# Kernel optimization log

Hardware: AMD Instinct MI355X
Metric: run time of the kernel (lower is better)

The kernel has to match this reference:

```python
import jax, jax.numpy as jnp
import numpy as np

NEG_SLOPE = 0.2


def gat_layer(x_src, x_dst, src, dst, W, a_src, a_dst, b, n_dst, H, C):
    # Linear transform: [Ns, H, C] / [Nd, H, C]
    h_s = (x_src @ W).reshape(-1, H, C)
    h_d = (x_dst @ W).reshape(-1, H, C)
    # Per-edge attention logits: a . [x_i || x_j] (x_i = dst/target, x_j = src)
    e = jnp.einsum('ehc,hc->eh', h_s[src], a_src) + jnp.einsum('ehc,hc->eh', h_d[dst], a_dst)
    e = jax.nn.leaky_relu(e, NEG_SLOPE)  # [E, H]
    # Segment softmax over destination neighborhoods
    m = jax.ops.segment_max(e, dst, num_segments=n_dst)          # [Nd, H]
    ex = jnp.exp(e - m[dst])
    denom = jax.ops.segment_sum(ex, dst, num_segments=n_dst)    # [Nd, H]
    alpha = ex / denom[dst]                                      # [E, H]
    # Weighted scatter-sum aggregation
    out = jax.ops.segment_sum(alpha[:, :, None] * h_s[src], dst, num_segments=n_dst)
    return out.reshape(n_dst, H * C) + b


def setup_inputs() -> dict:
    key = jax.random.key(0)
    ks = jax.random.split(key, 16)
    N, F_IN, OUT = 200000, 602, 41
    N1, N1D, E1 = 120000, 30000, 960000
    N2D, E2 = 6000, 192000
    s = 0.05
    return {
        'x': jax.random.normal(ks[0], (N, F_IN), jnp.float32),
        'n_id1': jax.random.randint(ks[1], (N1,), 0, N),
        'res_n_id1': jax.random.randint(ks[2], (N1D,), 0, N1),
        'edge_src1': jax.random.randint(ks[3], (E1,), 0, N1),
        'edge_dst1': jax.random.randint(ks[4], (E1,), 0, N1D),
        'res_n_id2': jax.random.randint(ks[5], (N2D,), 0, N1D),
        'edge_src2': jax.random.randint(ks[6], (E2,), 0, N1D),
        'edge_dst2': jax.random.randint(ks[7], (E2,), 0, N2D),
        'W1': jax.random.normal(ks[8], (F_IN, 64), jnp.float32) * s,
        'att_src1': jax.random.normal(ks[9], (8, 8), jnp.float32) * s,
        'att_dst1': jax.random.normal(ks[10], (8, 8), jnp.float32) * s,
        'bias1': jax.random.normal(ks[11], (64,), jnp.float32) * s,
        'W2': jax.random.normal(ks[12], (64, OUT), jnp.float32) * s,
        'att_src2': jax.random.normal(ks[13], (1, OUT), jnp.float32) * s,
        'att_dst2': jax.random.normal(ks[14], (1, OUT), jnp.float32) * s,
        'bias2': jax.random.normal(ks[15], (OUT,), jnp.float32) * s,
    }


def reference(x, n_id1, res_n_id1, edge_src1, edge_dst1, res_n_id2, edge_src2,
              edge_dst2, W1, att_src1, att_dst1, bias1, W2, att_src2, att_dst2, bias2):
    # Block 1: gather frontier, GATConv(in -> 8, heads=8, concat) -> [N1D, 64]
    h = x[n_id1]
    h = gat_layer(h, h[res_n_id1], edge_src1, edge_dst1,
                  W1, att_src1, att_dst1, bias1, res_n_id1.shape[0], 8, 8)
    h = jax.nn.elu(h)
    # (dropout p=0.6 is identity in eval mode)
    # Block 2: GATConv(64 -> out, heads=1) -> [N2D, out]
    h = gat_layer(h, h[res_n_id2], edge_src2, edge_dst2,
                  W2, att_src2, att_dst2, bias2, res_n_id2.shape[0], 1, W2.shape[1])
    return jax.nn.log_softmax(h, axis=1)
```

## Files before the change

### kernel.cpp

```cpp
#include <hip/hip_runtime.h>
#include <hip/hip_bf16.h>
#include <math.h>

typedef __attribute__((ext_vector_type(8))) short short8;
typedef __attribute__((ext_vector_type(4))) float float4v;

__device__ __forceinline__ float wave_max64(float v) {
#pragma unroll
  for (int o = 32; o > 0; o >>= 1) v = fmaxf(v, __shfl_xor(v, o));
  return v;
}
__device__ __forceinline__ float wave_sum64(float v) {
#pragma unroll
  for (int o = 32; o > 0; o >>= 1) v += __shfl_xor(v, o);
  return v;
}
__device__ __forceinline__ float lrelu02(float v) { return v > 0.f ? v : 0.2f * v; }
__device__ __forceinline__ short bf16_rne(float f) {
  unsigned u = __builtin_bit_cast(unsigned, f);
  unsigned r = (u + 0x7FFFu + ((u >> 16) & 1u)) >> 16;
  return (short)r;
}

__global__ void hist_prepack_kernel(const int* __restrict__ dst1, const int* __restrict__ dst2,
                                    int* __restrict__ counts, const float* __restrict__ W,
                                    short* __restrict__ Wp, int E1, int E2, int N1D, int nbE) {
  int b = blockIdx.x;
  if (b < nbE) {
    int e = b * 256 + threadIdx.x;
    if (e < E1) atomicAdd(&counts[dst1[e]], 1);
    else if (e < E1 + E2) atomicAdd(&counts[N1D + dst2[e - E1]], 1);
  } else {
    int idx = (b - nbE) * 256 + threadIdx.x;
    if (idx >= 19 * 4 * 64) return;
    int lane = idx & 63;
    int t = (idx >> 6) & 3;
    int s = idx >> 8;
    int quad = lane >> 4, n = t * 16 + (lane & 15);
    short8 v;
#pragma unroll
    for (int j = 0; j < 8; j++) {
      int k = s * 32 + quad * 8 + j;
      v[j] = (k < 602) ? bf16_rne(W[k * 64 + n]) : (short)0;
    }
    *((short8*)Wp + idx) = v;
  }
}

__global__ __launch_bounds__(256) void scan1_kernel(const int* __restrict__ counts,
                                                    int* __restrict__ offs,
                                                    int* __restrict__ bsum, int n) {
  __shared__ int ws[4], wpre[4];
  int tid = threadIdx.x, lane = tid & 63, w = tid >> 6;
  int i = blockIdx.x * 256 + tid;
  int v = (i < n) ? counts[i] : 0;
  int x = v;
#pragma unroll
  for (int o = 1; o < 64; o <<= 1) {
    int y = __shfl_up(x, o);
    if (lane >= o) x += y;
  }
  if (lane == 63) ws[w] = x;
  __syncthreads();
  if (tid == 0) {
    int run = 0;
#pragma unroll
    for (int k = 0; k < 4; k++) { wpre[k] = run; run += ws[k]; }
    bsum[blockIdx.x] = run;
  }
  __syncthreads();
  if (i < n) offs[i] = x - v + wpre[w];
}

__global__ __launch_bounds__(256) void scan2_kernel(int* __restrict__ bsum, int nb) {
  __shared__ int ws[4], wpre[4];
  int tid = threadIdx.x, lane = tid & 63, w = tid >> 6;
  int v = (tid < nb) ? bsum[tid] : 0;
  int x = v;
#pragma unroll
  for (int o = 1; o < 64; o <<= 1) {
    int y = __shfl_up(x, o);
    if (lane >= o) x += y;
  }
  if (lane == 63) ws[w] = x;
  __syncthreads();
  if (tid == 0) {
    int run = 0;
#pragma unroll
    for (int k = 0; k < 4; k++) { wpre[k] = run; run += ws[k]; }
  }
  __syncthreads();
  if (tid < nb) bsum[tid] = x - v + wpre[w];
}

__global__ __launch_bounds__(256) void scan3_kernel(int* __restrict__ offs,
                                                    const int* __restrict__ bsum,
                                                    int n, int etot) {
  int i = blockIdx.x * 256 + threadIdx.x;
  if (i < n) offs[i] += bsum[blockIdx.x];
  if (i == 0) offs[n] = etot;
}

__global__ void scatter_kernel(const int* __restrict__ dst1, const int* __restrict__ src1,
                               const int* __restrict__ dst2, const int* __restrict__ src2,
                               const int* __restrict__ offs, int* __restrict__ cursor,
                               int* __restrict__ epay, int E1, int E2, int N1D) {
  int e = blockIdx.x * blockDim.x + threadIdx.x;
  if (e < E1) {
    int d = dst1[e];
    int pos = offs[d] + atomicAdd(&cursor[d], 1);
    epay[pos] = src1[e];
  } else if (e < E1 + E2) {
    int e2 = e - E1;
    int d = N1D + dst2[e2];
    int pos = offs[d] + atomicAdd(&cursor[d], 1);
    epay[pos] = src2[e2];
  }
}

__global__ __launch_bounds__(256) void gemm1_mfma_kernel(const float* __restrict__ x,
                                                         const int* __restrict__ n_id,
                                                         const short* __restrict__ Wp,
                                                         float* __restrict__ out, int M) {
  constexpr int K = 602, NSTEP = 19;
  int tid = threadIdx.x;
  int wid = tid >> 6, lane = tid & 63;
  int quad = lane >> 4, mrow = lane & 15;
  int r = blockIdx.x * 64 + wid * 16 + mrow;
  int grow = n_id[r < M ? r : M - 1];
  const float* xrow = x + (size_t)grow * K;
  float4v acc[4] = {{0.f, 0.f, 0.f, 0.f}, {0.f, 0.f, 0.f, 0.f},
                    {0.f, 0.f, 0.f, 0.f}, {0.f, 0.f, 0.f, 0.f}};
  for (int s = 0; s < NSTEP; s++) {
    int k0 = s * 32 + quad * 8;
    float af[8];
    if (k0 + 8 <= K) {
#pragma unroll
      for (int j = 0; j < 8; j += 2) {
        float2 v = *(const float2*)(xrow + k0 + j);
        af[j] = v.x;
        af[j + 1] = v.y;
      }
    } else {
#pragma unroll
      for (int j = 0; j < 8; j++) af[j] = (k0 + j < K) ? xrow[k0 + j] : 0.f;
    }
    short8 a;
#pragma unroll
    for (int j = 0; j < 8; j++) a[j] = bf16_rne(af[j]);
    const short8* wp = (const short8*)Wp + (size_t)s * 256 + lane;
#pragma unroll
    for (int t = 0; t < 4; t++) {
      short8 b = wp[t * 64];
      acc[t] = __builtin_amdgcn_mfma_f32_16x16x32_bf16(a, b, acc[t], 0, 0, 0);
    }
  }
  int rb = blockIdx.x * 64 + wid * 16;
#pragma unroll
  for (int t = 0; t < 4; t++) {
#pragma unroll
    for (int j = 0; j < 4; j++) {
      int rr = rb + quad * 4 + j;
      if (rr < M) out[(size_t)rr * 64 + t * 16 + mrow] = acc[t][j];
    }
  }
}

__global__ void attn_src1_kernel(const float* __restrict__ hs1, const float* __restrict__ a,
                                 float* __restrict__ s, int N) {
  int t = blockIdx.x * blockDim.x + threadIdx.x;
  if (t >= N * 8) return;
  int i = t >> 3, h = t & 7;
  const float* p = hs1 + (size_t)i * 64 + h * 8;
  const float* q = a + h * 8;
  float acc = 0.f;
#pragma unroll
  for (int j = 0; j < 8; j++) acc += p[j] * q[j];
  s[t] = acc;
}

__global__ __launch_bounds__(256) void agg1_kernel(
    const int* __restrict__ offs, const int* __restrict__ srcs,
    const float* __restrict__ s_src, const int* __restrict__ res,
    const float* __restrict__ ad, const float* __restrict__ hs1,
    const float* __restrict__ bias, float* __restrict__ h1, int n_dst) {
  int wid = (blockIdx.x * blockDim.x + threadIdx.x) >> 6;
  if (wid >= n_dst) return;
  int lane = threadIdx.x & 63;
  int h = lane >> 3;
  int node = res[wid];
  float v = hs1[(size_t)node * 64 + lane] * ad[lane];
  v += __shfl_xor(v, 1);
  v += __shfl_xor(v, 2);
  v += __shfl_xor(v, 4);
  float sd = v;
  int beg = offs[wid], end = offs[wid + 1];
  float mx = -1e30f, den = 0.f, acc = 0.f;
  for (int i = beg; i < end; i += 8) {
    int m = end - i; if (m > 8) m = 8;
    int sr[8]; float ss[8], row[8];
#pragma unroll
    for (int j = 0; j < 8; j++) sr[j] = srcs[i + (j < m ? j : 0)];
#pragma unroll
    for (int j = 0; j < 8; j++) ss[j] = s_src[sr[j] * 8 + h];
#pragma unroll
    for (int j = 0; j < 8; j++) row[j] = hs1[(size_t)sr[j] * 64 + lane];
    float p[8];
#pragma unroll
    for (int j = 0; j < 8; j++) p[j] = (j < m) ? lrelu02(ss[j] + sd) : -1e30f;
    float bm = mx;
#pragma unroll
    for (int j = 0; j < 8; j++) bm = fmaxf(bm, p[j]);
    float scale = __expf(mx - bm);
    den *= scale;
    acc *= scale;
#pragma unroll
    for (int j = 0; j < 8; j++) {
      float w = __expf(p[j] - bm);
      den += w;
      acc += w * row[j];
    }
    mx = bm;
  }
  float val = (end > beg) ? acc / den : 0.f;
  val += bias[lane];
  val = val > 0.f ? val : __expf(val) - 1.f;
  h1[(size_t)wid * 64 + lane] = val;
}

__global__ __launch_bounds__(256) void gemm2_kernel(const float* __restrict__ h1,
                                                    const float* __restrict__ W2,
                                                    const float* __restrict__ a_src,
                                                    float* __restrict__ hs2,
                                                    float* __restrict__ ssrc, int M) {
  constexpr int C = 41;
  __shared__ float Ws[64 * C];
  for (int i = threadIdx.x; i < 64 * C; i += 256) Ws[i] = W2[i];
  __syncthreads();
  int lane = threadIdx.x & 63;
  int r = blockIdx.x * 4 + (threadIdx.x >> 6);
  if (r >= M) return;
  const float* row = h1 + (size_t)r * 64;
  float acc = 0.f;
  if (lane < C) {
#pragma unroll 8
    for (int k = 0; k < 64; k++) acc += row[k] * Ws[k * C + lane];
  }
  float t = (lane < C) ? acc * a_src[lane] : 0.f;
  t = wave_sum64(t);
  if (lane == 0) ssrc[r] = t;
  if (lane < C) hs2[(size_t)r * C + lane] = acc;
}

__global__ __launch_bounds__(256) void agg2_kernel(
    const int* __restrict__ offs, const int* __restrict__ srcs,
    const float* __restrict__ s_src, const int* __restrict__ res,
    const float* __restrict__ ad, const float* __restrict__ hs2,
    const float* __restrict__ bias, float* __restrict__ out, int n_dst) {
  constexpr int C = 41;
  int wid = (blockIdx.x * blockDim.x + threadIdx.x) >> 6;
  if (wid >= n_dst) return;
  int lane = threadIdx.x & 63;
  bool act = lane < C;
  int node = res[wid];
  float dv = act ? hs2[(size_t)node * C + lane] * ad[lane] : 0.f;
  float sd = wave_sum64(dv);
  int beg = offs[wid], end = offs[wid + 1];
  float mx = -1e30f, den = 0.f, acc = 0.f;
  for (int i = beg; i < end; i += 8) {
    int m = end - i; if (m > 8) m = 8;
    int sr[8]; float ss[8], row[8];
#pragma unroll
    for (int j = 0; j < 8; j++) sr[j] = srcs[i + (j < m ? j : 0)];
#pragma unroll
    for (int j = 0; j < 8; j++) ss[j] = s_src[sr[j]];
#pragma unroll
    for (int j = 0; j < 8; j++) row[j] = act ? hs2[(size_t)sr[j] * C + lane] : 0.f;
    float p[8];
#pragma unroll
    for (int j = 0; j < 8; j++) p[j] = (j < m) ? lrelu02(ss[j] + sd) : -1e30f;
    float bm = mx;
#pragma unroll
    for (int j = 0; j < 8; j++) bm = fmaxf(bm, p[j]);
    float scale = __expf(mx - bm);
    den *= scale;
    acc *= scale;
#pragma unroll
    for (int j = 0; j < 8; j++) {
      float w = __expf(p[j] - bm);
      den += w;
      acc += w * row[j];
    }
    mx = bm;
  }
  float val = (end > beg) ? acc / den : 0.f;
  if (act) val += bias[lane];
  float lv = act ? val : -1e30f;
  float m2 = wave_max64(lv);
  float ex = act ? __expf(val - m2) : 0.f;
  float ssum = wave_sum64(ex);
  if (act) out[(size_t)wid * C + lane] = val - m2 - __logf(ssum);
}

extern "C" void kernel_launch(void* const* d_in, const int* in_sizes, int n_in,
                              void* d_out, int out_size, void* d_ws, size_t ws_size,
                              hipStream_t stream) {
  const float* x    = (const float*)d_in[0];
  const int* n_id1  = (const int*)d_in[1];
  const int* res1   = (const int*)d_in[2];
  const int* esrc1  = (const int*)d_in[3];
  const int* edst1  = (const int*)d_in[4];
  const int* res2   = (const int*)d_in[5];
  const int* esrc2  = (const int*)d_in[6];
  const int* edst2  = (const int*)d_in[7];
  const float* W1   = (const float*)d_in[8];
  const float* as1  = (const float*)d_in[9];
  const float* ad1  = (const float*)d_in[10];
  const float* b1   = (const float*)d_in[11];
  const float* W2   = (const float*)d_in[12];
  const float* as2  = (const float*)d_in[13];
  const float* ad2  = (const float*)d_in[14];
  const float* b2   = (const float*)d_in[15];
  float* out = (float*)d_out;

  const int N1  = in_sizes[1];
  const int N1D = in_sizes[2];
  const int E1  = in_sizes[3];
  const int N2D = in_sizes[5];
  const int E2  = in_sizes[6];
  const int NTOT = N1D + N2D;
  const int ETOT = E1 + E2;

  char* w = (char*)d_ws;
  size_t off = 0;
  auto alloc = [&](size_t bytes) -> void* {
    void* p = (void*)(w + off);
    off += (bytes + 255) & ~(size_t)255;
    return p;
  };
  float* hs1   = (float*)alloc((size_t)N1 * 64 * 4);
  float* ssrc1 = (float*)alloc((size_t)N1 * 8 * 4);
  float* h1    = (float*)alloc((size_t)N1D * 64 * 4);
  float* hs2   = (float*)alloc((size_t)N1D * 41 * 4);
  float* ssrc2 = (float*)alloc((size_t)N1D * 4);
  int* counts  = (int*)alloc((size_t)2 * NTOT * 4);
  int* cursor  = counts + NTOT;
  int* offs    = (int*)alloc((size_t)(NTOT + 1) * 4);
  int* bsum    = (int*)alloc((size_t)256 * 4);
  int* epay    = (int*)alloc((size_t)ETOT * 4);
  short* Wp    = (short*)alloc((size_t)19 * 4 * 64 * 8 * 2);
  (void)ws_size; (void)n_in; (void)out_size;

  hipMemsetAsync(counts, 0, (size_t)2 * NTOT * 4, stream);

  const int nbE = (ETOT + 255) / 256;
  const int nb = (NTOT + 255) / 256;
  hist_prepack_kernel<<<nbE + 19, 256, 0, stream>>>(edst1, edst2, counts, W1, Wp, E1, E2, N1D, nbE);
  scan1_kernel<<<nb, 256, 0, stream>>>(counts, offs, bsum, NTOT);
  scan2_kernel<<<1, 256, 0, stream>>>(bsum, nb);
  scan3_kernel<<<nb, 256, 0, stream>>>(offs, bsum, NTOT, ETOT);
  scatter_kernel<<<nbE, 256, 0, stream>>>(edst1, esrc1, edst2, esrc2, offs, cursor, epay, E1, E2, N1D);

  gemm1_mfma_kernel<<<(N1 + 63) / 64, 256, 0, stream>>>(x, n_id1, Wp, hs1, N1);
  attn_src1_kernel<<<(N1 * 8 + 255) / 256, 256, 0, stream>>>(hs1, as1, ssrc1, N1);
  agg1_kernel<<<(N1D + 3) / 4, 256, 0, stream>>>(offs, epay, ssrc1, res1, ad1, hs1, b1, h1, N1D);

  gemm2_kernel<<<(N1D + 3) / 4, 256, 0, stream>>>(h1, W2, as2, hs2, ssrc2, N1D);
  agg2_kernel<<<(N2D + 3) / 4, 256, 0, stream>>>(offs + N1D, epay, ssrc2, res2, ad2, hs2, b2, out, N2D);
}
```

Before: 837.5 us.

## Fuse scatter into GEMM1 launch, attention logits into GEMM1, GEMM2 into agg1

The CSR scatter now runs as extra blocks inside the GEMM1 launch, so both proceed concurrently. The per-head source attention logits are computed from the MFMA accumulators through shuffle reductions, which removes the separate attn_src1 pass that re-read hs1. The layer-2 linear transform and its logit are moved into agg1's epilogue through shared memory, which removes the h1 buffer round trip and one launch. In exchange, agg1 loads all of W2 into shared memory in every block (about 10KB each), which may reduce occupancy.

```diff
diff --git a/kernel.cpp b/kernel.cpp
--- a/kernel.cpp
+++ b/kernel.cpp
@@ -101,27 +101,28 @@
   if (i == 0) offs[n] = etot;
 }
 
-__global__ void scatter_kernel(const int* __restrict__ dst1, const int* __restrict__ src1,
-                               const int* __restrict__ dst2, const int* __restrict__ src2,
-                               const int* __restrict__ offs, int* __restrict__ cursor,
-                               int* __restrict__ epay, int E1, int E2, int N1D) {
-  int e = blockIdx.x * blockDim.x + threadIdx.x;
-  if (e < E1) {
-    int d = dst1[e];
-    int pos = offs[d] + atomicAdd(&cursor[d], 1);
-    epay[pos] = src1[e];
-  } else if (e < E1 + E2) {
-    int e2 = e - E1;
-    int d = N1D + dst2[e2];
-    int pos = offs[d] + atomicAdd(&cursor[d], 1);
-    epay[pos] = src2[e2];
-  }
-}
-
-__global__ __launch_bounds__(256) void gemm1_mfma_kernel(const float* __restrict__ x,
-                                                         const int* __restrict__ n_id,
-                                                         const short* __restrict__ Wp,
-                                                         float* __restrict__ out, int M) {
+__global__ __launch_bounds__(256) void gemm1_fused_kernel(
+    const float* __restrict__ x, const int* __restrict__ n_id,
+    const short* __restrict__ Wp, const float* __restrict__ as1,
+    float* __restrict__ out, float* __restrict__ ssrc1, int M, int nbG,
+    const int* __restrict__ dst1, const int* __restrict__ src1,
+    const int* __restrict__ dst2, const int* __restrict__ src2,
+    const int* __restrict__ offs, int* __restrict__ cursor,
+    int* __restrict__ epay, int E1, int E2, int N1D) {
+  if (blockIdx.x >= nbG) {
+    int e = (blockIdx.x - nbG) * 256 + threadIdx.x;
+    if (e < E1) {
+      int d = dst1[e];
+      int pos = offs[d] + atomicAdd(&cursor[d], 1);
+      epay[pos] = src1[e];
+    } else if (e < E1 + E2) {
+      int e2 = e - E1;
+      int d = N1D + dst2[e2];
+      int pos = offs[d] + atomicAdd(&cursor[d], 1);
+      epay[pos] = src2[e2];
+    }
+    return;
+  }
   constexpr int K = 602, NSTEP = 19;
   int tid = threadIdx.x;
   int wid = tid >> 6, lane = tid & 63;
@@ -164,29 +165,41 @@
       if (rr < M) out[(size_t)rr * 64 + t * 16 + mrow] = acc[t][j];
     }
   }
-}
-
-__global__ void attn_src1_kernel(const float* __restrict__ hs1, const float* __restrict__ a,
-                                 float* __restrict__ s, int N) {
-  int t = blockIdx.x * blockDim.x + threadIdx.x;
-  if (t >= N * 8) return;
-  int i = t >> 3, h = t & 7;
-  const float* p = hs1 + (size_t)i * 64 + h * 8;
-  const float* q = a + h * 8;
-  float acc = 0.f;
-#pragma unroll
-  for (int j = 0; j < 8; j++) acc += p[j] * q[j];
-  s[t] = acc;
+  float afv[4];
+#pragma unroll
+  for (int t = 0; t < 4; t++) afv[t] = as1[t * 16 + mrow];
+#pragma unroll
+  for (int t = 0; t < 4; t++) {
+#pragma unroll
+    for (int j = 0; j < 4; j++) {
+      float v = acc[t][j] * afv[t];
+      v += __shfl_xor(v, 1);
+      v += __shfl_xor(v, 2);
+      v += __shfl_xor(v, 4);
+      if ((lane & 7) == 0) {
+        int rr = rb + quad * 4 + j;
+        if (rr < M) ssrc1[rr * 8 + t * 2 + ((lane >> 3) & 1)] = v;
+      }
+    }
+  }
 }
 
 __global__ __launch_bounds__(256) void agg1_kernel(
     const int* __restrict__ offs, const int* __restrict__ srcs,
     const float* __restrict__ s_src, const int* __restrict__ res,
     const float* __restrict__ ad, const float* __restrict__ hs1,
-    const float* __restrict__ bias, float* __restrict__ h1, int n_dst) {
+    const float* __restrict__ bias, const float* __restrict__ W2,
+    const float* __restrict__ as2, float* __restrict__ hs2,
+    float* __restrict__ ssrc2, int n_dst) {
+  constexpr int C = 41;
+  __shared__ float Ws[64 * C];
+  __shared__ float rowsh[4][64];
+  for (int i = threadIdx.x; i < 64 * C; i += 256) Ws[i] = W2[i];
+  __syncthreads();
   int wid = (blockIdx.x * blockDim.x + threadIdx.x) >> 6;
   if (wid >= n_dst) return;
   int lane = threadIdx.x & 63;
+  int w = threadIdx.x >> 6;
   int h = lane >> 3;
   int node = res[wid];
   float v = hs1[(size_t)node * 64 + lane] * ad[lane];
@@ -216,40 +229,25 @@
     acc *= scale;
 #pragma unroll
     for (int j = 0; j < 8; j++) {
-      float w = __expf(p[j] - bm);
-      den += w;
-      acc += w * row[j];
+      float w2 = __expf(p[j] - bm);
+      den += w2;
+      acc += w2 * row[j];
     }
     mx = bm;
   }
   float val = (end > beg) ? acc / den : 0.f;
   val += bias[lane];
   val = val > 0.f ? val : __expf(val) - 1.f;
-  h1[(size_t)wid * 64 + lane] = val;
-}
-
-__global__ __launch_bounds__(256) void gemm2_kernel(const float* __restrict__ h1,
-                                                    const float* __restrict__ W2,
-                                                    const float* __restrict__ a_src,
-                                                    float* __restrict__ hs2,
-                                                    float* __restrict__ ssrc, int M) {
-  constexpr int C = 41;
-  __shared__ float Ws[64 * C];
-  for (int i = threadIdx.x; i < 64 * C; i += 256) Ws[i] = W2[i];
-  __syncthreads();
-  int lane = threadIdx.x & 63;
-  int r = blockIdx.x * 4 + (threadIdx.x >> 6);
-  if (r >= M) return;
-  const float* row = h1 + (size_t)r * 64;
-  float acc = 0.f;
+  rowsh[w][lane] = val;
+  float acc2 = 0.f;
   if (lane < C) {
 #pragma unroll 8
-    for (int k = 0; k < 64; k++) acc += row[k] * Ws[k * C + lane];
-  }
-  float t = (lane < C) ? acc * a_src[lane] : 0.f;
-  t = wave_sum64(t);
-  if (lane == 0) ssrc[r] = t;
-  if (lane < C) hs2[(size_t)r * C + lane] = acc;
+    for (int k = 0; k < 64; k++) acc2 += rowsh[w][k] * Ws[k * C + lane];
+  }
+  float tt = (lane < C) ? acc2 * as2[lane] : 0.f;
+  tt = wave_sum64(tt);
+  if (lane == 0) ssrc2[wid] = tt;
+  if (lane < C) hs2[(size_t)wid * C + lane] = acc2;
 }
 
 __global__ __launch_bounds__(256) void agg2_kernel(
@@ -340,7 +338,6 @@
   };
   float* hs1   = (float*)alloc((size_t)N1 * 64 * 4);
   float* ssrc1 = (float*)alloc((size_t)N1 * 8 * 4);
-  float* h1    = (float*)alloc((size_t)N1D * 64 * 4);
   float* hs2   = (float*)alloc((size_t)N1D * 41 * 4);
   float* ssrc2 = (float*)alloc((size_t)N1D * 4);
   int* counts  = (int*)alloc((size_t)2 * NTOT * 4);
@@ -359,12 +356,13 @@
   scan1_kernel<<<nb, 256, 0, stream>>>(counts, offs, bsum, NTOT);
   scan2_kernel<<<1, 256, 0, stream>>>(bsum, nb);
   scan3_kernel<<<nb, 256, 0, stream>>>(offs, bsum, NTOT, ETOT);
-  scatter_kernel<<<nbE, 256, 0, stream>>>(edst1, esrc1, edst2, esrc2, offs, cursor, epay, E1, E2, N1D);
-
-  gemm1_mfma_kernel<<<(N1 + 63) / 64, 256, 0, stream>>>(x, n_id1, Wp, hs1, N1);
-  attn_src1_kernel<<<(N1 * 8 + 255) / 256, 256, 0, stream>>>(hs1, as1, ssrc1, N1);
-  agg1_kernel<<<(N1D + 3) / 4, 256, 0, stream>>>(offs, epay, ssrc1, res1, ad1, hs1, b1, h1, N1D);
-
-  gemm2_kernel<<<(N1D + 3) / 4, 256, 0, stream>>>(h1, W2, as2, hs2, ssrc2, N1D);
+
+  const int nbG = (N1 + 63) / 64;
+  gemm1_fused_kernel<<<nbG + nbE, 256, 0, stream>>>(
+      x, n_id1, Wp, as1, hs1, ssrc1, N1, nbG,
+      edst1, esrc1, edst2, esrc2, offs, cursor, epay, E1, E2, N1D);
+  agg1_kernel<<<(N1D + 3) / 4, 256, 0, stream>>>(offs, epay, ssrc1, res1, ad1, hs1, b1,
+                                                 W2, as2, hs2, ssrc2, N1D);
+
   agg2_kernel<<<(N2D + 3) / 4, 256, 0, stream>>>(offs + N1D, epay, ssrc2, res2, ad2, hs2, b2, out, N2D);
 }
```

Result: faster. 811.7 us (-3.1%).
